# Optimization experiments

Hardware: AMD Instinct MI355X
Metric: run time of the kernel (lower is better)

The kernel has to match this reference:

```python
import jax, jax.numpy as jnp
import numpy as np

LATENT = 128
HIDDEN = 512
N_STEPS = 50
BATCH = 8192


def _linear_init(k, fan_in, fan_out):
    kw, kb = jax.random.split(k)
    lim = 1.0 / np.sqrt(fan_in)
    W = jax.random.uniform(kw, (fan_in, fan_out), minval=-lim, maxval=lim, dtype=jnp.float32)
    b = jax.random.uniform(kb, (fan_out,), minval=-lim, maxval=lim, dtype=jnp.float32)
    return W, b


def setup_inputs() -> dict:
    key = jax.random.key(0)
    ks = jax.random.split(key, 6)
    in_dim = 2 * LATENT + 2  # x + condition + t_emb + target_emb
    W1, b1 = _linear_init(ks[0], in_dim, HIDDEN)
    W2, b2 = _linear_init(ks[1], HIDDEN, HIDDEN)
    W3, b3 = _linear_init(ks[2], HIDDEN, HIDDEN)
    W4, b4 = _linear_init(ks[3], HIDDEN, LATENT)
    condition = jax.random.normal(ks[4], (BATCH, LATENT), dtype=jnp.float32)
    x_init = jax.random.normal(ks[5], (BATCH, LATENT), dtype=jnp.float32)
    return dict(condition=condition, x_init=x_init,
                W1=W1, b1=b1, W2=W2, b2=b2, W3=W3, b3=b3, W4=W4, b4=b4,
                target_survival=1)


def reference(condition, x_init, W1, b1, W2, b2, W3, b3, W4, b4, target_survival):
    n_steps = N_STEPS
    betas = jnp.linspace(1e-4, 0.02, n_steps).astype(x_init.dtype)
    alphas = 1.0 - betas
    alphas_cumprod = jnp.cumprod(alphas)
    batch = condition.shape[0]
    # target = zeros if target_survival else ones (static python scalar)
    target = jnp.full((batch, 1), 0.0 if target_survival else 1.0, dtype=x_init.dtype)
    noise_key = jax.random.key(42)

    def step(x, t):
        t_emb = jnp.full((batch, 1), 1.0, x.dtype) * (t.astype(x.dtype) / n_steps)
        inp = jnp.concatenate([x, condition, t_emb, target], axis=-1)  # [B, 2L+2]
        h = jax.nn.gelu(inp @ W1 + b1, approximate=False)
        h = jax.nn.gelu(h @ W2 + b2, approximate=False)
        h = jax.nn.gelu(h @ W3 + b3, approximate=False)
        noise_pred = h @ W4 + b4  # [B, L]
        noise = jax.random.normal(jax.random.fold_in(noise_key, t), x.shape, x.dtype)
        noise = jnp.where(t > 0, noise, jnp.zeros_like(noise))  # no noise at t=0
        beta_t = betas[t]
        x = (x - beta_t / jnp.sqrt(1.0 - alphas_cumprod[t]) * noise_pred) / jnp.sqrt(alphas[t])
        x = x + jnp.sqrt(beta_t) * noise
        return x, None

    ts = jnp.arange(n_steps - 1, -1, -1)  # reversed(range(n_steps))
    x_final, _ = jax.lax.scan(step, x_init, ts)
    return x_final
```

## Files before the change

kernel.cpp:

```cpp
#include <hip/hip_runtime.h>
#include <stdint.h>
#include <stddef.h>


typedef __bf16 bf16;
typedef __bf16 bf16x4 __attribute__((ext_vector_type(4)));
typedef __bf16 bf16x8 __attribute__((ext_vector_type(8)));
typedef float  floatx4 __attribute__((ext_vector_type(4)));

#define NSTEPS    50
#define WG_ROWS   32
#define XB_STRIDE 136
#define H_STRIDE  520

__device__ __forceinline__ uint32_t rotl32(uint32_t x, int r) {
  return (x << r) | (x >> (32 - r));
}

__device__ __forceinline__ void threefry2x32(uint32_t k0, uint32_t k1,
                                             uint32_t x0, uint32_t x1,
                                             uint32_t& o0, uint32_t& o1) {
  uint32_t k2 = k0 ^ k1 ^ 0x1BD11BDAu;
  x0 += k0; x1 += k1;
#define TF_R(R) { x0 += x1; x1 = rotl32(x1, R); x1 ^= x0; }
  TF_R(13) TF_R(15) TF_R(26) TF_R(6)
  x0 += k1; x1 += k2 + 1u;
  TF_R(17) TF_R(29) TF_R(16) TF_R(24)
  x0 += k2; x1 += k0 + 2u;
  TF_R(13) TF_R(15) TF_R(26) TF_R(6)
  x0 += k0; x1 += k1 + 3u;
  TF_R(17) TF_R(29) TF_R(16) TF_R(24)
  x0 += k1; x1 += k2 + 4u;
  TF_R(13) TF_R(15) TF_R(26) TF_R(6)
  x0 += k2; x1 += k0 + 5u;
#undef TF_R
  o0 = x0; o1 = x1;
}

__device__ __forceinline__ float erfinv_xla_bl(float x) {
  float w = -0.6931471805599453f * __builtin_amdgcn_logf(fmaf(-x, x, 1.0f));
  float wa = w - 2.5f;
  float pa = 2.81022636e-08f;
  pa = fmaf(pa, wa, 3.43273939e-07f);
  pa = fmaf(pa, wa, -3.5233877e-06f);
  pa = fmaf(pa, wa, -4.39150654e-06f);
  pa = fmaf(pa, wa, 0.00021858087f);
  pa = fmaf(pa, wa, -0.00125372503f);
  pa = fmaf(pa, wa, -0.00417768164f);
  pa = fmaf(pa, wa, 0.246640727f);
  pa = fmaf(pa, wa, 1.50140941f);
  float wb = __builtin_amdgcn_sqrtf(w) - 3.0f;
  float pb = -0.000200214257f;
  pb = fmaf(pb, wb, 0.000100950558f);
  pb = fmaf(pb, wb, 0.00134934322f);
  pb = fmaf(pb, wb, -0.00367342844f);
  pb = fmaf(pb, wb, 0.00573950773f);
  pb = fmaf(pb, wb, -0.0076224613f);
  pb = fmaf(pb, wb, 0.00943887047f);
  pb = fmaf(pb, wb, 1.00167406f);
  pb = fmaf(pb, wb, 2.83297682f);
  float p = (w < 5.0f) ? pa : pb;
  return p * x;
}

__device__ __forceinline__ float gelu_fast(float x) {
  float z  = x * 0.7071067811865475f;
  float az = fabsf(z);
  float t  = __builtin_amdgcn_rcpf(fmaf(0.3275911f, az, 1.0f));
  float p  = fmaf(1.061405429f, t, -1.453152027f);
  p = fmaf(p, t, 1.421413741f);
  p = fmaf(p, t, -0.284496736f);
  p = fmaf(p, t, 0.254829592f);
  p *= t;
  float e  = __builtin_amdgcn_exp2f(az * az * -1.4426950408889634f);
  float er = fmaf(-p, e, 1.0f);
  er = copysignf(er, z);
  return 0.5f * x * (1.0f + er);
}

template<int KSTEPS, int BSTRIDE, int UNROLL>
__device__ __forceinline__ void gemm2t(const bf16* __restrict__ h_lds,
                                       const bf16* __restrict__ A_pk,
                                       int lane, floatx4 (&acc)[2][2]) {
  const int nrow = lane & 15, q = lane >> 4;
  const bf16* b0 = h_lds + nrow * BSTRIDE + q * 8;
  const bf16* a0 = A_pk + lane * 8;
#pragma unroll UNROLL
  for (int ks = 0; ks < KSTEPS; ++ks) {
    bf16x8 bf0 = *(const bf16x8*)(b0 + ks * 32);
    bf16x8 bf1 = *(const bf16x8*)(b0 + 16 * BSTRIDE + ks * 32);
    bf16x8 aA  = *(const bf16x8*)(a0 + ks * 512);
    bf16x8 aB  = *(const bf16x8*)(a0 + (KSTEPS + ks) * 512);
    acc[0][0] = __builtin_amdgcn_mfma_f32_16x16x32_bf16(aA, bf0, acc[0][0], 0, 0, 0);
    acc[0][1] = __builtin_amdgcn_mfma_f32_16x16x32_bf16(aA, bf1, acc[0][1], 0, 0, 0);
    acc[1][0] = __builtin_amdgcn_mfma_f32_16x16x32_bf16(aB, bf0, acc[1][0], 0, 0, 0);
    acc[1][1] = __builtin_amdgcn_mfma_f32_16x16x32_bf16(aB, bf1, acc[1][1], 0, 0, 0);
  }
}

template<int KSTEPS, int BSTRIDE>
__device__ __forceinline__ void gemm1t(const bf16* __restrict__ h_lds,
                                       const bf16* __restrict__ A_pk,
                                       int lane, floatx4& acc) {
  const int nrow = lane & 15, q = lane >> 4;
  const bf16* b0 = h_lds + nrow * BSTRIDE + q * 8;
  const bf16* a0 = A_pk + lane * 8;
#pragma unroll 4
  for (int ks = 0; ks < KSTEPS; ++ks) {
    bf16x8 bfr = *(const bf16x8*)(b0 + ks * 32);
    bf16x8 af  = *(const bf16x8*)(a0 + ks * 512);
    acc = __builtin_amdgcn_mfma_f32_16x16x32_bf16(af, bfr, acc, 0, 0, 0);
  }
}

__global__ void diff_prep(const float* __restrict__ W1, const float* __restrict__ b1,
                          const float* __restrict__ W2, const float* __restrict__ W3,
                          const float* __restrict__ W4, const int* __restrict__ tsurv,
                          bf16* __restrict__ w1p, bf16* __restrict__ w1cp,
                          bf16* __restrict__ w2p, bf16* __restrict__ w3p,
                          bf16* __restrict__ w4p,
                          float* __restrict__ eb1, uint32_t* __restrict__ fk,
                          float* __restrict__ cst) {
  const int tid = blockIdx.x * blockDim.x + threadIdx.x;
  const int nth = gridDim.x * blockDim.x;
  for (int i = tid; i < 512 * 128; i += nth) {
    int j = i & 7, lane = (i >> 3) & 63, ks = (i >> 9) & 3, ntg = i >> 11;
    int n = ntg * 16 + (lane & 15);
    int k = ks * 32 + (lane >> 4) * 8 + j;
    w1p[i]  = (bf16)W1[k * 512 + n];
    w1cp[i] = (bf16)W1[(128 + k) * 512 + n];
  }
  for (int i = tid; i < 512 * 512; i += nth) {
    int j = i & 7, lane = (i >> 3) & 63, ks = (i >> 9) & 15, ntg = i >> 13;
    int n = ntg * 16 + (lane & 15);
    int k = ks * 32 + (lane >> 4) * 8 + j;
    w2p[i] = (bf16)W2[k * 512 + n];
    w3p[i] = (bf16)W3[k * 512 + n];
  }
  for (int i = tid; i < 128 * 512; i += nth) {
    int j = i & 7, lane = (i >> 3) & 63, ks = (i >> 9) & 15, ntg = i >> 13;
    int n = ntg * 16 + (lane & 15);
    int k = ks * 32 + (lane >> 4) * 8 + j;
    w4p[i] = (bf16)W4[k * 128 + n];
  }
  const float tgt = (tsurv[0] != 0) ? 0.0f : 1.0f;
  for (int i = tid; i < NSTEPS * 512; i += nth) {
    int t = i >> 9, n = i & 511;
    eb1[i] = b1[n] + ((float)t / 50.0f) * W1[256 * 512 + n] + tgt * W1[257 * 512 + n];
  }
  if (tid == 0) {
    float ac = 1.0f;
    for (int t = 0; t < NSTEPS; ++t) {
      float beta  = 1e-4f + (0.02f - 1e-4f) * ((float)t / 49.0f);
      float alpha = 1.0f - beta;
      ac *= alpha;
      cst[t]            = beta / sqrtf(1.0f - ac);
      cst[NSTEPS + t]   = 1.0f / sqrtf(alpha);
      cst[2*NSTEPS + t] = sqrtf(beta);
      uint32_t o0, o1;
      threefry2x32(0u, 42u, 0u, (uint32_t)t, o0, o1);
      fk[t] = o0; fk[NSTEPS + t] = o1;
    }
  }
}

__global__ __launch_bounds__(1024, 4) void diff_main(
    const float* __restrict__ cond, const float* __restrict__ xinit,
    const bf16* __restrict__ w1p, const bf16* __restrict__ w1cp,
    const bf16* __restrict__ w2p, const bf16* __restrict__ w3p,
    const bf16* __restrict__ w4p,
    const float* __restrict__ eb1, const float* __restrict__ b2,
    const float* __restrict__ b3, const float* __restrict__ b4,
    const uint32_t* __restrict__ fk, const float* __restrict__ cst,
    float* __restrict__ out) {
  __shared__ bf16 xb[WG_ROWS * XB_STRIDE];
  __shared__ bf16 hbA[WG_ROWS * H_STRIDE];
  __shared__ bf16 hbB[WG_ROWS * H_STRIDE];

  const int tid  = threadIdx.x;
  const int wave = tid >> 6;
  const int lane = tid & 63;
  const int nrow = lane & 15, q = lane >> 4;
  const int r0   = blockIdx.x * WG_ROWS;
  const int mc0  = wave * 32;
  const int qc   = q * 4;

  const int mtile4 = wave & 7;
  const int ntile4 = wave >> 3;
  const int n4     = ntile4 * 16 + nrow;
  const int xc0    = mtile4 * 16 + qc;

  {
    const int row = tid >> 5;
    const int c4  = (tid & 31) * 4;
    float4 a = *(const float4*)(xinit + (size_t)(r0 + row) * 128 + c4);
    float4 c = *(const float4*)(cond  + (size_t)(r0 + row) * 128 + c4);
    bf16x4 x4, c4v;
    x4[0] = (bf16)a.x; x4[1] = (bf16)a.y; x4[2] = (bf16)a.z; x4[3] = (bf16)a.w;
    c4v[0] = (bf16)c.x; c4v[1] = (bf16)c.y; c4v[2] = (bf16)c.z; c4v[3] = (bf16)c.w;
    *(bf16x4*)(xb  + row * XB_STRIDE + c4) = x4;
    *(bf16x4*)(hbA + row * H_STRIDE  + c4) = c4v;
  }
  float4 xreg = *(const float4*)(xinit + (size_t)(r0 + n4) * 128 + xc0);
  __syncthreads();

  floatx4 cpr[2][2] = {};
  gemm2t<4, H_STRIDE, 4>(hbA, w1cp + (wave * 2) * 4 * 512, lane, cpr);
  __syncthreads();

  for (int t = NSTEPS - 1; t >= 0; --t) {
    {
      floatx4 acc[2][2] = {};
      gemm2t<4, XB_STRIDE, 4>(xb, w1p + (wave * 2) * 4 * 512, lane, acc);
      const float* ebt = eb1 + t * 512;
#pragma unroll
      for (int mt = 0; mt < 2; ++mt) {
        const int col = mc0 + mt * 16 + qc;
        float4 bb = *(const float4*)(ebt + col);
#pragma unroll
        for (int nt = 0; nt < 2; ++nt) {
          bf16x4 g;
#pragma unroll
          for (int r = 0; r < 4; ++r)
            g[r] = (bf16)gelu_fast(acc[mt][nt][r] + cpr[mt][nt][r] + ((const float*)&bb)[r]);
          *(bf16x4*)(hbA + (nt * 16 + nrow) * H_STRIDE + col) = g;
        }
      }
    }
    __syncthreads();

    {
      floatx4 acc[2][2] = {};
      gemm2t<16, H_STRIDE, 4>(hbA, w2p + (wave * 2) * 16 * 512, lane, acc);
#pragma unroll
      for (int mt = 0; mt < 2; ++mt) {
        const int col = mc0 + mt * 16 + qc;
        float4 bb = *(const float4*)(b2 + col);
#pragma unroll
        for (int nt = 0; nt < 2; ++nt) {
          bf16x4 g;
#pragma unroll
          for (int r = 0; r < 4; ++r)
            g[r] = (bf16)gelu_fast(acc[mt][nt][r] + ((const float*)&bb)[r]);
          *(bf16x4*)(hbB + (nt * 16 + nrow) * H_STRIDE + col) = g;
        }
      }
    }
    __syncthreads();

    {
      floatx4 acc[2][2] = {};
      gemm2t<16, H_STRIDE, 4>(hbB, w3p + (wave * 2) * 16 * 512, lane, acc);
#pragma unroll
      for (int mt = 0; mt < 2; ++mt) {
        const int col = mc0 + mt * 16 + qc;
        float4 bb = *(const float4*)(b3 + col);
#pragma unroll
        for (int nt = 0; nt < 2; ++nt) {
          bf16x4 g;
#pragma unroll
          for (int r = 0; r < 4; ++r)
            g[r] = (bf16)gelu_fast(acc[mt][nt][r] + ((const float*)&bb)[r]);
          *(bf16x4*)(hbA + (nt * 16 + nrow) * H_STRIDE + col) = g;
        }
      }
    }
    __syncthreads();

    {
      floatx4 acc = {};
      gemm1t<16, H_STRIDE>(hbA + ntile4 * 16 * H_STRIDE,
                           w4p + mtile4 * 16 * 512, lane, acc);
      const float c1 = cst[t], c2 = cst[NSTEPS + t], c3 = cst[2 * NSTEPS + t];
      const uint32_t fk0 = fk[t], fk1 = fk[NSTEPS + t];
      const float zscale = (t > 0) ? 1.4142135381698608f : 0.0f;
      float4 bb = *(const float4*)(b4 + xc0);
      const uint32_t gbase = (uint32_t)(r0 + n4) * 128u + (uint32_t)xc0;
      bf16x4 xpk;
#pragma unroll
      for (int r = 0; r < 4; ++r) {
        float np = acc[r] + ((const float*)&bb)[r];
        uint32_t o0, o1;
        threefry2x32(fk0, fk1, 0u, gbase + (uint32_t)r, o0, o1);
        uint32_t bits = o0 ^ o1;
        float f01 = __uint_as_float((bits >> 9) | 0x3F800000u) - 1.0f;
        float u = fmaxf(-0.99999994f, fmaf(f01, 2.0f, -0.99999994f));
        float z = zscale * erfinv_xla_bl(u);
        float xn = (((float*)&xreg)[r] - c1 * np) * c2 + c3 * z;
        ((float*)&xreg)[r] = xn;
        xpk[r] = (bf16)xn;
      }
      *(bf16x4*)(xb + n4 * XB_STRIDE + xc0) = xpk;
    }
    __syncthreads();
  }

  *(float4*)(out + (size_t)(r0 + n4) * 128 + xc0) = xreg;
}

extern "C" void kernel_launch(void* const* d_in, const int* in_sizes, int n_in,
                              void* d_out, int out_size, void* d_ws, size_t ws_size,
                              hipStream_t stream) {
  const float* cond  = (const float*)d_in[0];
  const float* xinit = (const float*)d_in[1];
  const float* W1 = (const float*)d_in[2];
  const float* b1 = (const float*)d_in[3];
  const float* W2 = (const float*)d_in[4];
  const float* b2 = (const float*)d_in[5];
  const float* W3 = (const float*)d_in[6];
  const float* b3 = (const float*)d_in[7];
  const float* W4 = (const float*)d_in[8];
  const float* b4 = (const float*)d_in[9];
  const int* tsurv = (const int*)d_in[10];

  char* ws = (char*)d_ws;
  bf16* w1p  = (bf16*)(ws + 0);
  bf16* w1cp = (bf16*)(ws + 131072);
  bf16* w2p  = (bf16*)(ws + 262144);
  bf16* w3p  = (bf16*)(ws + 786432);
  bf16* w4p  = (bf16*)(ws + 1310720);
  float* eb1 = (float*)(ws + 1441792);
  uint32_t* fkp = (uint32_t*)(ws + 1544192);
  float* cstp = (float*)(ws + 1544704);

  diff_prep<<<1024, 256, 0, stream>>>(W1, b1, W2, W3, W4, tsurv,
                                      w1p, w1cp, w2p, w3p, w4p, eb1, fkp, cstp);
  diff_main<<<256, 1024, 0, stream>>>(cond, xinit, w1p, w1cp, w2p, w3p, w4p,
                                      eb1, b2, b3, b4, fkp, cstp, (float*)d_out);
}
```

Before: 984.9 us.

## Halve workgroup size to 512 threads, each wave computes two column panels

```diff
diff --git a/kernel.cpp b/kernel.cpp
--- a/kernel.cpp
+++ b/kernel.cpp
@@ -78,6 +78,8 @@
   return 0.5f * x * (1.0f + er);
 }
 
+#define MFMA16(a, b, c) __builtin_amdgcn_mfma_f32_16x16x32_bf16((a), (b), (c), 0, 0, 0)
+
 template<int KSTEPS, int BSTRIDE, int UNROLL>
 __device__ __forceinline__ void gemm2t(const bf16* __restrict__ h_lds,
                                        const bf16* __restrict__ A_pk,
@@ -91,25 +93,26 @@
     bf16x8 bf1 = *(const bf16x8*)(b0 + 16 * BSTRIDE + ks * 32);
     bf16x8 aA  = *(const bf16x8*)(a0 + ks * 512);
     bf16x8 aB  = *(const bf16x8*)(a0 + (KSTEPS + ks) * 512);
-    acc[0][0] = __builtin_amdgcn_mfma_f32_16x16x32_bf16(aA, bf0, acc[0][0], 0, 0, 0);
-    acc[0][1] = __builtin_amdgcn_mfma_f32_16x16x32_bf16(aA, bf1, acc[0][1], 0, 0, 0);
-    acc[1][0] = __builtin_amdgcn_mfma_f32_16x16x32_bf16(aB, bf0, acc[1][0], 0, 0, 0);
-    acc[1][1] = __builtin_amdgcn_mfma_f32_16x16x32_bf16(aB, bf1, acc[1][1], 0, 0, 0);
-  }
-}
-
-template<int KSTEPS, int BSTRIDE>
-__device__ __forceinline__ void gemm1t(const bf16* __restrict__ h_lds,
-                                       const bf16* __restrict__ A_pk,
-                                       int lane, floatx4& acc) {
+    acc[0][0] = MFMA16(aA, bf0, acc[0][0]);
+    acc[0][1] = MFMA16(aA, bf1, acc[0][1]);
+    acc[1][0] = MFMA16(aB, bf0, acc[1][0]);
+    acc[1][1] = MFMA16(aB, bf1, acc[1][1]);
+  }
+}
+
+__device__ __forceinline__ void gemm_l4(const bf16* __restrict__ h_lds,
+                                        const bf16* __restrict__ A_pk,
+                                        int lane, floatx4 (&acc4)[2]) {
   const int nrow = lane & 15, q = lane >> 4;
-  const bf16* b0 = h_lds + nrow * BSTRIDE + q * 8;
+  const bf16* b0 = h_lds + nrow * H_STRIDE + q * 8;
   const bf16* a0 = A_pk + lane * 8;
 #pragma unroll 4
-  for (int ks = 0; ks < KSTEPS; ++ks) {
-    bf16x8 bfr = *(const bf16x8*)(b0 + ks * 32);
+  for (int ks = 0; ks < 16; ++ks) {
+    bf16x8 bf0 = *(const bf16x8*)(b0 + ks * 32);
+    bf16x8 bf1 = *(const bf16x8*)(b0 + 16 * H_STRIDE + ks * 32);
     bf16x8 af  = *(const bf16x8*)(a0 + ks * 512);
-    acc = __builtin_amdgcn_mfma_f32_16x16x32_bf16(af, bfr, acc, 0, 0, 0);
+    acc4[0] = MFMA16(af, bf0, acc4[0]);
+    acc4[1] = MFMA16(af, bf1, acc4[1]);
   }
 }
 
@@ -164,7 +167,7 @@
   }
 }
 
-__global__ __launch_bounds__(1024, 4) void diff_main(
+__global__ __launch_bounds__(512, 2) void diff_main(
     const float* __restrict__ cond, const float* __restrict__ xinit,
     const bf16* __restrict__ w1p, const bf16* __restrict__ w1cp,
     const bf16* __restrict__ w2p, const bf16* __restrict__ w3p,
@@ -182,120 +185,149 @@
   const int lane = tid & 63;
   const int nrow = lane & 15, q = lane >> 4;
   const int r0   = blockIdx.x * WG_ROWS;
-  const int mc0  = wave * 32;
   const int qc   = q * 4;
-
-  const int mtile4 = wave & 7;
-  const int ntile4 = wave >> 3;
-  const int n4     = ntile4 * 16 + nrow;
-  const int xc0    = mtile4 * 16 + qc;
+  const int xc0  = wave * 16 + qc;
+
+  const bf16* w4base = w4p + wave * 16 * 512;
 
   {
-    const int row = tid >> 5;
-    const int c4  = (tid & 31) * 4;
-    float4 a = *(const float4*)(xinit + (size_t)(r0 + row) * 128 + c4);
-    float4 c = *(const float4*)(cond  + (size_t)(r0 + row) * 128 + c4);
-    bf16x4 x4, c4v;
-    x4[0] = (bf16)a.x; x4[1] = (bf16)a.y; x4[2] = (bf16)a.z; x4[3] = (bf16)a.w;
-    c4v[0] = (bf16)c.x; c4v[1] = (bf16)c.y; c4v[2] = (bf16)c.z; c4v[3] = (bf16)c.w;
-    *(bf16x4*)(xb  + row * XB_STRIDE + c4) = x4;
-    *(bf16x4*)(hbA + row * H_STRIDE  + c4) = c4v;
-  }
-  float4 xreg = *(const float4*)(xinit + (size_t)(r0 + n4) * 128 + xc0);
+    const int row = tid >> 4;
+    const int c0  = (tid & 15) * 8;
+    float4 a  = *(const float4*)(xinit + (size_t)(r0 + row) * 128 + c0);
+    float4 a2 = *(const float4*)(xinit + (size_t)(r0 + row) * 128 + c0 + 4);
+    float4 c  = *(const float4*)(cond  + (size_t)(r0 + row) * 128 + c0);
+    float4 c2 = *(const float4*)(cond  + (size_t)(r0 + row) * 128 + c0 + 4);
+    bf16x8 xs, cs;
+    xs[0] = (bf16)a.x;  xs[1] = (bf16)a.y;  xs[2] = (bf16)a.z;  xs[3] = (bf16)a.w;
+    xs[4] = (bf16)a2.x; xs[5] = (bf16)a2.y; xs[6] = (bf16)a2.z; xs[7] = (bf16)a2.w;
+    cs[0] = (bf16)c.x;  cs[1] = (bf16)c.y;  cs[2] = (bf16)c.z;  cs[3] = (bf16)c.w;
+    cs[4] = (bf16)c2.x; cs[5] = (bf16)c2.y; cs[6] = (bf16)c2.z; cs[7] = (bf16)c2.w;
+    *(bf16x8*)(xb  + row * XB_STRIDE + c0) = xs;
+    *(bf16x8*)(hbA + row * H_STRIDE  + c0) = cs;
+  }
+  float4 xregA = *(const float4*)(xinit + (size_t)(r0 + nrow)      * 128 + xc0);
+  float4 xregB = *(const float4*)(xinit + (size_t)(r0 + nrow + 16) * 128 + xc0);
   __syncthreads();
 
-  floatx4 cpr[2][2] = {};
-  gemm2t<4, H_STRIDE, 4>(hbA, w1cp + (wave * 2) * 4 * 512, lane, cpr);
+  floatx4 cpr[2][2][2] = {};
+#pragma unroll
+  for (int p = 0; p < 2; ++p)
+    gemm2t<4, H_STRIDE, 4>(hbA, w1cp + ((p * 8 + wave) * 2) * 4 * 512, lane, cpr[p]);
   __syncthreads();
 
   for (int t = NSTEPS - 1; t >= 0; --t) {
     {
-      floatx4 acc[2][2] = {};
-      gemm2t<4, XB_STRIDE, 4>(xb, w1p + (wave * 2) * 4 * 512, lane, acc);
       const float* ebt = eb1 + t * 512;
 #pragma unroll
-      for (int mt = 0; mt < 2; ++mt) {
-        const int col = mc0 + mt * 16 + qc;
-        float4 bb = *(const float4*)(ebt + col);
-#pragma unroll
-        for (int nt = 0; nt < 2; ++nt) {
-          bf16x4 g;
-#pragma unroll
-          for (int r = 0; r < 4; ++r)
-            g[r] = (bf16)gelu_fast(acc[mt][nt][r] + cpr[mt][nt][r] + ((const float*)&bb)[r]);
-          *(bf16x4*)(hbA + (nt * 16 + nrow) * H_STRIDE + col) = g;
+      for (int p = 0; p < 2; ++p) {
+        floatx4 acc[2][2] = {};
+        gemm2t<4, XB_STRIDE, 4>(xb, w1p + ((p * 8 + wave) * 2) * 4 * 512, lane, acc);
+        const int pc0 = (p * 8 + wave) * 32;
+#pragma unroll
+        for (int mt = 0; mt < 2; ++mt) {
+          const int col = pc0 + mt * 16 + qc;
+          float4 bb = *(const float4*)(ebt + col);
+#pragma unroll
+          for (int nt = 0; nt < 2; ++nt) {
+            bf16x4 g;
+#pragma unroll
+            for (int r = 0; r < 4; ++r)
+              g[r] = (bf16)gelu_fast(acc[mt][nt][r] + cpr[p][mt][nt][r] + ((const float*)&bb)[r]);
+            *(bf16x4*)(hbA + (nt * 16 + nrow) * H_STRIDE + col) = g;
+          }
         }
       }
     }
     __syncthreads();
 
     {
-      floatx4 acc[2][2] = {};
-      gemm2t<16, H_STRIDE, 4>(hbA, w2p + (wave * 2) * 16 * 512, lane, acc);
-#pragma unroll
-      for (int mt = 0; mt < 2; ++mt) {
-        const int col = mc0 + mt * 16 + qc;
-        float4 bb = *(const float4*)(b2 + col);
-#pragma unroll
-        for (int nt = 0; nt < 2; ++nt) {
-          bf16x4 g;
-#pragma unroll
-          for (int r = 0; r < 4; ++r)
-            g[r] = (bf16)gelu_fast(acc[mt][nt][r] + ((const float*)&bb)[r]);
-          *(bf16x4*)(hbB + (nt * 16 + nrow) * H_STRIDE + col) = g;
+#pragma unroll
+      for (int p = 0; p < 2; ++p) {
+        floatx4 acc[2][2] = {};
+        gemm2t<16, H_STRIDE, 4>(hbA, w2p + ((p * 8 + wave) * 2) * 16 * 512, lane, acc);
+        const int pc0 = (p * 8 + wave) * 32;
+#pragma unroll
+        for (int mt = 0; mt < 2; ++mt) {
+          const int col = pc0 + mt * 16 + qc;
+          float4 bb = *(const float4*)(b2 + col);
+#pragma unroll
+          for (int nt = 0; nt < 2; ++nt) {
+            bf16x4 g;
+#pragma unroll
+            for (int r = 0; r < 4; ++r)
+              g[r] = (bf16)gelu_fast(acc[mt][nt][r] + ((const float*)&bb)[r]);
+            *(bf16x4*)(hbB + (nt * 16 + nrow) * H_STRIDE + col) = g;
+          }
         }
       }
     }
     __syncthreads();
 
     {
-      floatx4 acc[2][2] = {};
-      gemm2t<16, H_STRIDE, 4>(hbB, w3p + (wave * 2) * 16 * 512, lane, acc);
-#pragma unroll
-      for (int mt = 0; mt < 2; ++mt) {
-        const int col = mc0 + mt * 16 + qc;
-        float4 bb = *(const float4*)(b3 + col);
-#pragma unroll
-        for (int nt = 0; nt < 2; ++nt) {
-          bf16x4 g;
-#pragma unroll
-          for (int r = 0; r < 4; ++r)
-            g[r] = (bf16)gelu_fast(acc[mt][nt][r] + ((const float*)&bb)[r]);
-          *(bf16x4*)(hbA + (nt * 16 + nrow) * H_STRIDE + col) = g;
+#pragma unroll
+      for (int p = 0; p < 2; ++p) {
+        floatx4 acc[2][2] = {};
+        gemm2t<16, H_STRIDE, 4>(hbB, w3p + ((p * 8 + wave) * 2) * 16 * 512, lane, acc);
+        const int pc0 = (p * 8 + wave) * 32;
+#pragma unroll
+        for (int mt = 0; mt < 2; ++mt) {
+          const int col = pc0 + mt * 16 + qc;
+          float4 bb = *(const float4*)(b3 + col);
+#pragma unroll
+          for (int nt = 0; nt < 2; ++nt) {
+            bf16x4 g;
+#pragma unroll
+            for (int r = 0; r < 4; ++r)
+              g[r] = (bf16)gelu_fast(acc[mt][nt][r] + ((const float*)&bb)[r]);
+            *(bf16x4*)(hbA + (nt * 16 + nrow) * H_STRIDE + col) = g;
+          }
         }
       }
     }
     __syncthreads();
 
     {
-      floatx4 acc = {};
-      gemm1t<16, H_STRIDE>(hbA + ntile4 * 16 * H_STRIDE,
-                           w4p + mtile4 * 16 * 512, lane, acc);
+      floatx4 acc4[2] = {};
+      gemm_l4(hbA, w4base, lane, acc4);
       const float c1 = cst[t], c2 = cst[NSTEPS + t], c3 = cst[2 * NSTEPS + t];
       const uint32_t fk0 = fk[t], fk1 = fk[NSTEPS + t];
       const float zscale = (t > 0) ? 1.4142135381698608f : 0.0f;
       float4 bb = *(const float4*)(b4 + xc0);
-      const uint32_t gbase = (uint32_t)(r0 + n4) * 128u + (uint32_t)xc0;
-      bf16x4 xpk;
-#pragma unroll
-      for (int r = 0; r < 4; ++r) {
-        float np = acc[r] + ((const float*)&bb)[r];
+      const uint32_t gbaseA = (uint32_t)(r0 + nrow) * 128u + (uint32_t)xc0;
+      const uint32_t gbaseB = (uint32_t)(r0 + nrow + 16) * 128u + (uint32_t)xc0;
+
+      float z[8];
+#pragma unroll
+      for (int r = 0; r < 8; ++r) {
+        const uint32_t gi = (r < 4) ? (gbaseA + (uint32_t)r) : (gbaseB + (uint32_t)(r - 4));
         uint32_t o0, o1;
-        threefry2x32(fk0, fk1, 0u, gbase + (uint32_t)r, o0, o1);
+        threefry2x32(fk0, fk1, 0u, gi, o0, o1);
         uint32_t bits = o0 ^ o1;
         float f01 = __uint_as_float((bits >> 9) | 0x3F800000u) - 1.0f;
         float u = fmaxf(-0.99999994f, fmaf(f01, 2.0f, -0.99999994f));
-        float z = zscale * erfinv_xla_bl(u);
-        float xn = (((float*)&xreg)[r] - c1 * np) * c2 + c3 * z;
-        ((float*)&xreg)[r] = xn;
-        xpk[r] = (bf16)xn;
-      }
-      *(bf16x4*)(xb + n4 * XB_STRIDE + xc0) = xpk;
+        z[r] = zscale * erfinv_xla_bl(u);
+      }
+
+      bf16x4 xpkA, xpkB;
+#pragma unroll
+      for (int r = 0; r < 4; ++r) {
+        float npA = acc4[0][r] + ((const float*)&bb)[r];
+        float xnA = (((float*)&xregA)[r] - c1 * npA) * c2 + c3 * z[r];
+        ((float*)&xregA)[r] = xnA;
+        xpkA[r] = (bf16)xnA;
+        float npB = acc4[1][r] + ((const float*)&bb)[r];
+        float xnB = (((float*)&xregB)[r] - c1 * npB) * c2 + c3 * z[r + 4];
+        ((float*)&xregB)[r] = xnB;
+        xpkB[r] = (bf16)xnB;
+      }
+      *(bf16x4*)(xb + nrow * XB_STRIDE + xc0)        = xpkA;
+      *(bf16x4*)(xb + (nrow + 16) * XB_STRIDE + xc0) = xpkB;
     }
     __syncthreads();
   }
 
-  *(float4*)(out + (size_t)(r0 + n4) * 128 + xc0) = xreg;
+  *(float4*)(out + (size_t)(r0 + nrow)      * 128 + xc0) = xregA;
+  *(float4*)(out + (size_t)(r0 + nrow + 16) * 128 + xc0) = xregB;
 }
 
 extern "C" void kernel_launch(void* const* d_in, const int* in_sizes, int n_in,
@@ -325,6 +357,6 @@
 
   diff_prep<<<1024, 256, 0, stream>>>(W1, b1, W2, W3, W4, tsurv,
                                       w1p, w1cp, w2p, w3p, w4p, eb1, fkp, cstp);
-  diff_main<<<256, 1024, 0, stream>>>(cond, xinit, w1p, w1cp, w2p, w3p, w4p,
-                                      eb1, b2, b3, b4, fkp, cstp, (float*)d_out);
-}
+  diff_main<<<256, 512, 0, stream>>>(cond, xinit, w1p, w1cp, w2p, w3p, w4p,
+                                     eb1, b2, b3, b4, fkp, cstp, (float*)d_out);
+}
```

Measured after the change: 1.028 ms. +4.4%, slower.
